# Optimization experiments

Hardware: AMD Instinct MI355X
Metric: run time of the kernel (lower is better)

Reference implementation:

```python
import jax, jax.numpy as jnp
import numpy as np

B, HOR, E, L = 16, 512, 1024, 12
ACT_NUM, DIM, ADIM = 10, 64, 10
N = 2 * HOR                      # backbone sequence length (test=False)
NPOS = 4 * (1 + HOR)             # wpe table size
D_IN = 3 + DIM * ACT_NUM + ADIM  # embed_transition input dim = 653


def setup_inputs() -> dict:
    key = jax.random.key(0)
    ks = jax.random.split(key, 12)
    s = lambda k, shape: (jax.random.normal(k, shape, jnp.float32) * 0.02)
    return {
        "action_set": jax.random.normal(ks[0], (B, ACT_NUM, DIM), jnp.float32),
        "context_rewards": jax.random.normal(ks[1], (B, HOR, 1), jnp.float32),
        "wpe": s(ks[2], (NPOS, E)),
        "W_emb": s(ks[3], (D_IN, E)),
        "b_emb": jnp.zeros((E,), jnp.float32),
        "Wq": s(ks[4], (L, E, E)),
        "Wk": s(ks[5], (L, E, E)),
        "Wv": s(ks[6], (L, E, E)),
        "ln1_g": jnp.ones((L, E), jnp.float32),
        "ln1_b": jnp.zeros((L, E), jnp.float32),
        "W1": s(ks[7], (L, E, E)),
        "b1": jnp.zeros((L, E), jnp.float32),
        "W2": s(ks[8], (L, E, E)),
        "b2": jnp.zeros((L, E), jnp.float32),
        "ln2_g": jnp.ones((L, E), jnp.float32),
        "ln2_b": jnp.zeros((L, E), jnp.float32),
        "W_pred": s(ks[9], (E, ADIM)),
        "b_pred": jnp.zeros((ADIM,), jnp.float32),
    }


def _layernorm(x, g, b, eps=1e-5):
    mu = x.mean(-1, keepdims=True)
    var = ((x - mu) ** 2).mean(-1, keepdims=True)
    return (x - mu) * jax.lax.rsqrt(var + eps) * g + b


def reference(action_set, context_rewards, wpe, W_emb, b_emb, Wq, Wk, Wv,
              ln1_g, ln1_b, W1, b1, W2, b2, ln2_g, ln2_b, W_pred, b_pred):
    batch = action_set.shape[0]
    hor = context_rewards.shape[1]
    n = 2 * hor
    # --- build interleaved sequence (outer Transformer glue) ---
    a = action_set.reshape(batch, 1, -1)                       # [B,1,DA]
    pair = jnp.concatenate([a, jnp.zeros_like(a)], axis=1)     # [B,2,DA]
    act_set_seq = jnp.tile(pair, (1, hor, 1))                  # [B,2H,DA]
    action_seq = jnp.zeros((batch, n, ADIM + 1), jnp.float32)
    one_seq = jnp.ones((batch, n, 1), jnp.float32)
    pos_seq = jnp.broadcast_to(
        jnp.arange(1, n + 1, dtype=jnp.float32).reshape(1, n, 1), (batch, n, 1))
    seq = jnp.concatenate([act_set_seq, action_seq, one_seq, pos_seq], axis=2)  # [B,N,D_IN]
    # --- DecoderTransformerBackbone ---
    Hs = seq @ W_emb + b_emb
    Hs = Hs + wpe[:n]                                          # positional embedding
    idx = jnp.arange(n)
    # normalized causal mask: row i has 1/(i+1) on j<=i, else 0
    mask = jnp.where(idx[:, None] >= idx[None, :],
                     1.0 / (idx[:, None].astype(jnp.float32) + 1.0), 0.0)
    for l in range(Wq.shape[0]):
        q = Hs @ Wq[l]
        k = Hs @ Wk[l]
        v = Hs @ Wv[l]
        attn = jax.nn.relu(jnp.einsum('bid,bjd->bij', q, k)) * mask
        Hs = Hs + jnp.einsum('bij,bjd->bid', attn, v)
        Hs = _layernorm(Hs, ln1_g[l], ln1_b[l])
        Hs = Hs + (jax.nn.relu(Hs @ W1[l] + b1[l]) @ W2[l] + b2[l])
        Hs = _layernorm(Hs, ln2_g[l], ln2_b[l])
    preds = Hs @ W_pred + b_pred                               # [B,N,ADIM]
    return preds[:, 0::2, :]                                   # [B,HOR,ADIM]
```

## Files before the change

### kernel.cpp

```cpp
#include <hip/hip_runtime.h>
#include <stdint.h>
#include <stddef.h>

#define E_DIM 1024
#define B_SZ  16
#define N_SEQ 1024
#define L_NUM 12
#define ACT_D 640
#define ADIM_ 10

typedef unsigned short u16;
typedef __attribute__((ext_vector_type(8))) short bf16x8;
typedef __attribute__((ext_vector_type(4))) float f32x4;

__device__ __forceinline__ u16 f2bf(float x) {
  union { float f; unsigned int u; } c; c.f = x;
  unsigned int r = c.u + 0x7fffu + ((c.u >> 16) & 1u);
  return (u16)(r >> 16);
}
__device__ __forceinline__ float bf2f(u16 h) {
  union { unsigned int u; float f; } c; c.u = ((unsigned int)h) << 16;
  return c.f;
}

struct us4 { u16 x, y, z, w; };

#define GLD16(gsrc, ldst) __builtin_amdgcn_global_load_lds( \
    (const __attribute__((address_space(1))) void*)(gsrc),  \
    (__attribute__((address_space(3))) void*)(ldst), 16, 0, 0)

#define BM 256
#define BK 32

template<int MODE, int EPI, int BNT>
__global__ __launch_bounds__(512)
void gemm_nt_mfma(const u16* __restrict__ Ah, const u16* __restrict__ Al,
                  const u16* __restrict__ Bh0, const u16* __restrict__ Bl0,
                  const u16* __restrict__ Bh1, const u16* __restrict__ Bl1,
                  float* __restrict__ Co,
                  u16* __restrict__ Ch0, u16* __restrict__ Cl0,
                  u16* __restrict__ Ch1, u16* __restrict__ Cl1,
                  const float* __restrict__ bias0, const float* __restrict__ bias1,
                  int K, int lda, int ldb, int ldc, int tilesN,
                  long long sA, long long sB, long long sC)
{
  constexpr int LA = BM * BK;
  constexpr int LB = BNT * BK;
  constexpr int BUFU = 2 * LA + 2 * LB;
  __shared__ u16 smem[2 * BUFU];

  constexpr int WAVE_R = (BNT == 256) ? 128 : 64;
  constexpr int WGC = BNT / 64;
  constexpr int MA = WAVE_R / 16;

  const int tid = threadIdx.x;
  const int bat = blockIdx.y;

  const u16* Bh = Bh0; const u16* Bl = Bl0;
  u16* Ch = Ch0; u16* Cl = Cl0;
  const float* bias = bias0;
  if (blockIdx.z) { Bh = Bh1; Bl = Bl1; Ch = Ch1; Cl = Cl1; bias = bias1; }

  Ah += bat * sA; Al += bat * sA;
  Bh += bat * sB; Bl += bat * sB;

  int bid;
  {
    const int nwg = gridDim.x;
    const int q = nwg >> 3, r = nwg & 7;
    const int xcd = blockIdx.x & 7, off = blockIdx.x >> 3;
    bid = ((xcd < r) ? xcd * (q + 1) : r * (q + 1) + (xcd - r) * q) + off;
  }

  int tm, tn;
  if (MODE == 1) {
    int t = bid, m = 0;
    while ((m + 1) * (m + 2) <= t) m++;
    tm = m; tn = t - m * (m + 1);
  } else {
    tm = bid / tilesN;
    tn = bid % tilesN;
  }
  int kend = K;
  if (MODE == 2) { int c = (tm + 1) * BM; kend = (c < K) ? c : K; }
  const int nk = kend / BK;

  const int ca0 = tid, ca1 = tid + 512;
  const int ra0 = ca0 >> 2, ra1 = ca1 >> 2;
  const int pa0 = ((ca0 & 3) ^ ((ra0 >> 1) & 3)) * 8;
  const int pa1 = ((ca1 & 3) ^ ((ra1 >> 1) & 3)) * 8;
  const int cb0 = tid, cb1 = tid + 512;
  const int rb0 = cb0 >> 2, rb1 = cb1 >> 2;
  const int pb0 = ((cb0 & 3) ^ ((rb0 >> 1) & 3)) * 8;
  const int pb1 = ((cb1 & 3) ^ ((rb1 >> 1) & 3)) * 8;

  const u16* gAh0 = Ah + (long long)(tm * BM + ra0) * lda + pa0;
  const u16* gAh1 = Ah + (long long)(tm * BM + ra1) * lda + pa1;
  const u16* gAl0 = Al + (long long)(tm * BM + ra0) * lda + pa0;
  const u16* gAl1 = Al + (long long)(tm * BM + ra1) * lda + pa1;
  const u16* gBh0 = Bh + (long long)(tn * BNT + rb0) * ldb + pb0;
  const u16* gBl0 = Bl + (long long)(tn * BNT + rb0) * ldb + pb0;
  const u16* gBh1 = Bh + (long long)(tn * BNT + rb1) * ldb + pb1;
  const u16* gBl1 = Bl + (long long)(tn * BNT + rb1) * ldb + pb1;
  const int oa0 = ca0 * 8, oa1 = ca1 * 8, ob0 = cb0 * 8, ob1 = cb1 * 8;

  auto stage = [&](int buf) {
    u16* base = smem + buf * BUFU;
    GLD16(gAh0, base + oa0);
    GLD16(gAh1, base + oa1);
    GLD16(gAl0, base + LA + oa0);
    GLD16(gAl1, base + LA + oa1);
    GLD16(gBh0, base + 2 * LA + ob0);
    GLD16(gBl0, base + 2 * LA + LB + ob0);
    if (BNT == 256) {
      GLD16(gBh1, base + 2 * LA + ob1);
      GLD16(gBl1, base + 2 * LA + LB + ob1);
    }
    gAh0 += BK; gAh1 += BK; gAl0 += BK; gAl1 += BK;
    gBh0 += BK; gBl0 += BK;
    if (BNT == 256) { gBh1 += BK; gBl1 += BK; }
  };

  const int lane = tid & 63;
  const int w = tid >> 6;
  const int wr = w / WGC, wc = w % WGC;
  const int fr = lane & 15;
  const int kq = (lane >> 4) * 8;
  const int sa = ((fr >> 1) & 3) << 3;
  const int aoff = ((wr * WAVE_R + fr) * BK + kq) ^ sa;
  const int boff = ((wc * 64 + fr) * BK + kq) ^ sa;

  f32x4 acc[MA][4];
  #pragma unroll
  for (int m = 0; m < MA; m++)
    #pragma unroll
    for (int n = 0; n < 4; n++) acc[m][n] = (f32x4){0.f, 0.f, 0.f, 0.f};

  stage(0);
  asm volatile("s_waitcnt vmcnt(0)" ::: "memory");
  __builtin_amdgcn_s_barrier();

  for (int t = 0; t < nk; t++) {
    if (t + 1 < nk) stage((t + 1) & 1);
    const u16* sb = smem + (t & 1) * BUFU;

    bf16x8 ah[MA], al[MA], bh[4], bl[4];
    #pragma unroll
    for (int m = 0; m < MA; m++) ah[m] = *(const bf16x8*)(sb + aoff + m * (16 * BK));
    #pragma unroll
    for (int n = 0; n < 4; n++) bh[n] = *(const bf16x8*)(sb + 2 * LA + boff + n * (16 * BK));
    __builtin_amdgcn_s_setprio(1);
    #pragma unroll
    for (int m = 0; m < MA; m++)
      #pragma unroll
      for (int n = 0; n < 4; n++)
        acc[m][n] = __builtin_amdgcn_mfma_f32_16x16x32_bf16(ah[m], bh[n], acc[m][n], 0, 0, 0);
    __builtin_amdgcn_s_setprio(0);
    #pragma unroll
    for (int m = 0; m < MA; m++) al[m] = *(const bf16x8*)(sb + LA + aoff + m * (16 * BK));
    __builtin_amdgcn_s_setprio(1);
    #pragma unroll
    for (int m = 0; m < MA; m++)
      #pragma unroll
      for (int n = 0; n < 4; n++)
        acc[m][n] = __builtin_amdgcn_mfma_f32_16x16x32_bf16(al[m], bh[n], acc[m][n], 0, 0, 0);
    __builtin_amdgcn_s_setprio(0);
    #pragma unroll
    for (int n = 0; n < 4; n++) bl[n] = *(const bf16x8*)(sb + 2 * LA + LB + boff + n * (16 * BK));
    __builtin_amdgcn_s_setprio(1);
    #pragma unroll
    for (int m = 0; m < MA; m++)
      #pragma unroll
      for (int n = 0; n < 4; n++)
        acc[m][n] = __builtin_amdgcn_mfma_f32_16x16x32_bf16(ah[m], bl[n], acc[m][n], 0, 0, 0);
    __builtin_amdgcn_s_setprio(0);

    if (t + 1 < nk) {
      asm volatile("s_waitcnt vmcnt(0)" ::: "memory");
      __builtin_amdgcn_s_barrier();
    }
  }

  if (Co) Co += bat * sC;
  if (Ch) { Ch += bat * sC; Cl += bat * sC; }
  #pragma unroll
  for (int m = 0; m < MA; m++) {
    #pragma unroll
    for (int r = 0; r < 4; r++) {
      const long long row = (long long)tm * BM + wr * WAVE_R + m * 16 + (lane >> 4) * 4 + r;
      #pragma unroll
      for (int n = 0; n < 4; n++) {
        const long long col = (long long)tn * BNT + wc * 64 + n * 16 + (lane & 15);
        float v = acc[m][n][r];
        if (EPI == 2) { v += bias[col]; v = v > 0.f ? v : 0.f; }
        if (EPI == 4) { v += bias[col]; }
        if (EPI == 3) {
          v = v > 0.f ? v : 0.f;
          v = (col <= row) ? v / (float)(row + 1) : 0.f;
        }
        const long long idx = row * (long long)ldc + col;
        if (EPI == 0 || EPI == 4) {
          Co[idx] = v;
        } else {
          u16 h = f2bf(v);
          Ch[idx] = h;
          Cl[idx] = f2bf(v - bf2f(h));
        }
      }
    }
  }
}

struct TP3 {
  const float* s0; const float* s1; const float* s2;
  u16* h0; u16* l0; u16* h1; u16* l1; u16* h2; u16* l2;
};

__global__ __launch_bounds__(256)
void transpose_split3(TP3 p)
{
  __shared__ float tile[32][33];
  const float* src; u16* dh; u16* dl;
  if (blockIdx.z == 0)      { src = p.s0; dh = p.h0; dl = p.l0; }
  else if (blockIdx.z == 1) { src = p.s1; dh = p.h1; dl = p.l1; }
  else                      { src = p.s2; dh = p.h2; dl = p.l2; }
  const int c0 = blockIdx.x * 32, r0 = blockIdx.y * 32;
  const int tx = threadIdx.x & 31, ty = threadIdx.x >> 5;
  #pragma unroll
  for (int i = ty; i < 32; i += 8)
    tile[i][tx] = src[(long long)(r0 + i) * E_DIM + c0 + tx];
  __syncthreads();
  #pragma unroll
  for (int i = ty; i < 32; i += 8) {
    const float v = tile[tx][i];
    const u16 h = f2bf(v);
    const long long idx = (long long)(c0 + i) * E_DIM + r0 + tx;
    dh[idx] = h;
    dl[idx] = f2bf(v - bf2f(h));
  }
}

__global__ __launch_bounds__(256)
void resid_ln(u16* __restrict__ hh, u16* __restrict__ hl,
              const float* __restrict__ delta,
              const float* __restrict__ g, const float* __restrict__ bta)
{
  __shared__ float red[8];
  const long long row = blockIdx.x;
  u16* hp = hh + row * E_DIM;
  u16* lp = hl + row * E_DIM;
  const float* dp = delta + row * E_DIM;
  const int tid = threadIdx.x;
  const int e = tid * 4;

  us4 hv = *(const us4*)(hp + e);
  us4 lv = *(const us4*)(lp + e);
  float4 d = *(const float4*)(dp + e);
  float x0 = bf2f(hv.x) + bf2f(lv.x) + d.x;
  float x1 = bf2f(hv.y) + bf2f(lv.y) + d.y;
  float x2 = bf2f(hv.z) + bf2f(lv.z) + d.z;
  float x3 = bf2f(hv.w) + bf2f(lv.w) + d.w;
  float s = x0 + x1 + x2 + x3;
  float q = x0 * x0 + x1 * x1 + x2 * x2 + x3 * x3;
  #pragma unroll
  for (int o = 32; o > 0; o >>= 1) { s += __shfl_down(s, o); q += __shfl_down(q, o); }
  const int lane = tid & 63, wv = tid >> 6;
  if (lane == 0) { red[wv] = s; red[wv + 4] = q; }
  __syncthreads();
  const float st = red[0] + red[1] + red[2] + red[3];
  const float qt = red[4] + red[5] + red[6] + red[7];
  const float mu = st * (1.0f / E_DIM);
  const float var = qt * (1.0f / E_DIM) - mu * mu;
  const float rstd = rsqrtf(var + 1e-5f);

  float4 gg = *(const float4*)(g + e);
  float4 bb = *(const float4*)(bta + e);
  float y0 = (x0 - mu) * rstd * gg.x + bb.x;
  float y1 = (x1 - mu) * rstd * gg.y + bb.y;
  float y2 = (x2 - mu) * rstd * gg.z + bb.z;
  float y3 = (x3 - mu) * rstd * gg.w + bb.w;

  us4 ho, lo;
  ho.x = f2bf(y0); lo.x = f2bf(y0 - bf2f(ho.x));
  ho.y = f2bf(y1); lo.y = f2bf(y1 - bf2f(ho.y));
  ho.z = f2bf(y2); lo.z = f2bf(y2 - bf2f(ho.z));
  ho.w = f2bf(y3); lo.w = f2bf(y3 - bf2f(ho.w));
  *(us4*)(hp + e) = ho;
  *(us4*)(lp + e) = lo;
}

__global__ __launch_bounds__(256)
void emb_dot(const float* __restrict__ act, const float* __restrict__ Wemb,
             float* __restrict__ Aemb)
{
  const int e = blockIdx.x * 256 + threadIdx.x;
  const int b = blockIdx.y;
  const float* ab = act + b * ACT_D;
  float s = 0.f;
  for (int d = 0; d < ACT_D; d++)
    s = fmaf(ab[d], Wemb[(long long)d * E_DIM + e], s);
  Aemb[b * E_DIM + e] = s;
}

__global__ __launch_bounds__(256)
void emb_fill(const float* __restrict__ Aemb, const float* __restrict__ Wemb,
              const float* __restrict__ bemb, const float* __restrict__ wpe,
              u16* __restrict__ oh, u16* __restrict__ ol)
{
  const int i = blockIdx.x, b = blockIdx.y;
  const int e = threadIdx.x * 4;
  float4 a;
  if ((i & 1) == 0) a = *(const float4*)(Aemb + b * E_DIM + e);
  else { a.x = 0.f; a.y = 0.f; a.z = 0.f; a.w = 0.f; }
  float4 be = *(const float4*)(bemb + e);
  float4 w1 = *(const float4*)(Wemb + 651LL * E_DIM + e);
  float4 w2 = *(const float4*)(Wemb + 652LL * E_DIM + e);
  float4 pw = *(const float4*)(wpe + (long long)i * E_DIM + e);
  const float pos = (float)(i + 1);
  float y0 = a.x + be.x + w1.x + pos * w2.x + pw.x;
  float y1 = a.y + be.y + w1.y + pos * w2.y + pw.y;
  float y2 = a.z + be.z + w1.z + pos * w2.z + pw.z;
  float y3 = a.w + be.w + w1.w + pos * w2.w + pw.w;
  const long long row = (long long)b * N_SEQ + i;

  us4 ho, lo;
  ho.x = f2bf(y0); lo.x = f2bf(y0 - bf2f(ho.x));
  ho.y = f2bf(y1); lo.y = f2bf(y1 - bf2f(ho.y));
  ho.z = f2bf(y2); lo.z = f2bf(y2 - bf2f(ho.z));
  ho.w = f2bf(y3); lo.w = f2bf(y3 - bf2f(ho.w));
  *(us4*)(oh + row * E_DIM + e) = ho;
  *(us4*)(ol + row * E_DIM + e) = lo;
}

__global__ __launch_bounds__(256)
void pred_k(const u16* __restrict__ hh, const u16* __restrict__ hl,
            const float* __restrict__ Wp, const float* __restrict__ bp,
            float* __restrict__ out)
{
  __shared__ float part[4][ADIM_];
  const int h = blockIdx.x, b = blockIdx.y;
  const long long row = (long long)b * N_SEQ + 2 * h;
  const u16* xh = hh + row * E_DIM;
  const u16* xl = hl + row * E_DIM;
  float acc[ADIM_];
  #pragma unroll
  for (int a = 0; a < ADIM_; a++) acc[a] = 0.f;
  for (int e = threadIdx.x; e < E_DIM; e += 256) {
    const float xv = bf2f(xh[e]) + bf2f(xl[e]);
    const float* wq = Wp + e * ADIM_;
    #pragma unroll
    for (int a = 0; a < ADIM_; a++) acc[a] = fmaf(xv, wq[a], acc[a]);
  }
  const int lane = threadIdx.x & 63, wv = threadIdx.x >> 6;
  #pragma unroll
  for (int a = 0; a < ADIM_; a++)
    #pragma unroll
    for (int o = 32; o > 0; o >>= 1) acc[a] += __shfl_down(acc[a], o);
  if (lane == 0)
    #pragma unroll
    for (int a = 0; a < ADIM_; a++) part[wv][a] = acc[a];
  __syncthreads();
  if (threadIdx.x < ADIM_) {
    const int a = threadIdx.x;
    out[((long long)b * (N_SEQ / 2) + h) * ADIM_ + a] =
        part[0][a] + part[1][a] + part[2][a] + part[3][a] + bp[a];
  }
}

__global__ __launch_bounds__(256)
void fill_sentinel(float* p, int n, float v)
{
  int i = blockIdx.x * 256 + threadIdx.x;
  if (i < n) p[i] = v;
}

extern "C" void kernel_launch(void* const* d_in, const int* in_sizes, int n_in,
                              void* d_out, int out_size, void* d_ws, size_t ws_size,
                              hipStream_t stream)
{
  const float* act  = (const float*)d_in[0];
  const float* wpe  = (const float*)d_in[2];
  const float* Wemb = (const float*)d_in[3];
  const float* bemb = (const float*)d_in[4];
  const float* Wq   = (const float*)d_in[5];
  const float* Wk   = (const float*)d_in[6];
  const float* Wv   = (const float*)d_in[7];
  const float* ln1g = (const float*)d_in[8];
  const float* ln1b = (const float*)d_in[9];
  const float* W1   = (const float*)d_in[10];
  const float* b1   = (const float*)d_in[11];
  const float* W2   = (const float*)d_in[12];
  const float* b2   = (const float*)d_in[13];
  const float* ln2g = (const float*)d_in[14];
  const float* ln2b = (const float*)d_in[15];
  const float* Wp   = (const float*)d_in[16];
  const float* bp   = (const float*)d_in[17];
  float* out = (float*)d_out;

  const long long sQ = (long long)N_SEQ * E_DIM;
  const long long sE = (long long)E_DIM * E_DIM;

  auto need = [&](int G) -> size_t {
    return (size_t)G * sQ * 16 + (size_t)sE * 12
         + (size_t)G * E_DIM * 4 + (size_t)(1 << 20);
  };
  int G = 16;
  while (G > 1 && need(G) > ws_size) G >>= 1;
  if (need(G) > ws_size || d_ws == nullptr || G < 8) {
    fill_sentinel<<<dim3((out_size + 255) / 256), 256, 0, stream>>>(out, out_size, 1.0e7f);
    return;
  }

  char* ws = (char*)d_ws;
  size_t off = 0;
  auto alloc = [&](size_t bytes) -> void* {
    void* p = ws + off;
    off += (bytes + 255) & ~(size_t)255;
    return p;
  };
  u16* hsh = (u16*)alloc((size_t)G * sQ * 2);
  u16* hsl = (u16*)alloc((size_t)G * sQ * 2);
  u16* qh  = (u16*)alloc((size_t)G * sQ * 2);
  u16* ql  = (u16*)alloc((size_t)G * sQ * 2);
  char* kreg = (char*)alloc((size_t)G * sQ * 4);
  u16* kh = (u16*)kreg;
  u16* kl = kh + (size_t)G * sQ;
  float* dbuf = (float*)kreg;
  u16* sh_ = (u16*)alloc((size_t)G * sQ * 2);
  u16* sl_ = (u16*)alloc((size_t)G * sQ * 2);
  u16* wAh = (u16*)alloc((size_t)sE * 2);
  u16* wAl = (u16*)alloc((size_t)sE * 2);
  u16* wBh = (u16*)alloc((size_t)sE * 2);
  u16* wBl = (u16*)alloc((size_t)sE * 2);
  u16* wCh = (u16*)alloc((size_t)sE * 2);
  u16* wCl = (u16*)alloc((size_t)sE * 2);
  float* Aemb = (float*)alloc((size_t)G * E_DIM * 4);

  const bool wide = (G >= 16);
  const int triS = 20;

  const dim3 gqk((G * N_SEQ / BM) * (E_DIM / 256), 1, 2);
  const dim3 gsq(triS, G, 1);
  const dim3 gm256((G * N_SEQ / BM) * (E_DIM / 256), 1, 1);
  const dim3 gm128((G * N_SEQ / BM) * (E_DIM / 128), 1, 1);
  const dim3 gv256((N_SEQ / BM) * (E_DIM / 256), G, 1);
  const dim3 gv128((N_SEQ / BM) * (E_DIM / 128), G, 1);

  for (int g0 = 0; g0 < B_SZ; g0 += G) {
    emb_dot<<<dim3(E_DIM / 256, G), 256, 0, stream>>>(act + (long long)g0 * ACT_D, Wemb, Aemb);
    emb_fill<<<dim3(N_SEQ, G), 256, 0, stream>>>(Aemb, Wemb, bemb, wpe, hsh, hsl);

    for (int l = 0; l < L_NUM; l++) {
      const long long wof = (long long)l * sE;
      const long long bof = (long long)l * E_DIM;

      TP3 t2 = {Wq + wof, Wk + wof, Wq + wof, wAh, wAl, wBh, wBl, wAh, wAl};
      transpose_split3<<<dim3(32, 32, 2), 256, 0, stream>>>(t2);
      gemm_nt_mfma<0, 1, 256><<<gqk, 512, 0, stream>>>(hsh, hsl, wAh, wAl, wBh, wBl,
          nullptr, qh, ql, kh, kl, nullptr, nullptr,
          E_DIM, E_DIM, E_DIM, E_DIM, E_DIM / 256, 0, 0, 0);

      TP3 t3 = {Wv + wof, W1 + wof, W2 + wof, wAh, wAl, wBh, wBl, wCh, wCl};
      transpose_split3<<<dim3(32, 32, 3), 256, 0, stream>>>(t3);

      gemm_nt_mfma<1, 3, 128><<<gsq, 512, 0, stream>>>(qh, ql, kh, kl, kh, kl,
          nullptr, sh_, sl_, sh_, sl_, nullptr, nullptr,
          E_DIM, E_DIM, E_DIM, N_SEQ, 0, sQ, sQ, sQ);

      if (wide)
        gemm_nt_mfma<0, 1, 256><<<gv256, 512, 0, stream>>>(wAh, wAl, hsh, hsl, hsh, hsl,
            nullptr, qh, ql, qh, ql, nullptr, nullptr,
            E_DIM, E_DIM, E_DIM, N_SEQ, E_DIM / 256, 0, sQ, sQ);
      else
        gemm_nt_mfma<0, 1, 128><<<gv128, 512, 0, stream>>>(wAh, wAl, hsh, hsl, hsh, hsl,
            nullptr, qh, ql, qh, ql, nullptr, nullptr,
            E_DIM, E_DIM, E_DIM, N_SEQ, E_DIM / 128, 0, sQ, sQ);

      if (wide)
        gemm_nt_mfma<2, 0, 256><<<gv256, 512, 0, stream>>>(sh_, sl_, qh, ql, qh, ql,
            dbuf, nullptr, nullptr, nullptr, nullptr, nullptr, nullptr,
            N_SEQ, N_SEQ, N_SEQ, E_DIM, E_DIM / 256, sQ, sQ, sQ);
      else
        gemm_nt_mfma<2, 0, 128><<<gv128, 512, 0, stream>>>(sh_, sl_, qh, ql, qh, ql,
            dbuf, nullptr, nullptr, nullptr, nullptr, nullptr, nullptr,
            N_SEQ, N_SEQ, N_SEQ, E_DIM, E_DIM / 128, sQ, sQ, sQ);

      resid_ln<<<dim3(G * N_SEQ), 256, 0, stream>>>(hsh, hsl, dbuf,
          ln1g + bof, ln1b + bof);

      if (wide)
        gemm_nt_mfma<0, 2, 256><<<gm256, 512, 0, stream>>>(hsh, hsl, wBh, wBl, wBh, wBl,
            nullptr, qh, ql, qh, ql, b1 + bof, b1 + bof,
            E_DIM, E_DIM, E_DIM, E_DIM, E_DIM / 256, 0, 0, 0);
      else
        gemm_nt_mfma<0, 2, 128><<<gm128, 512, 0, stream>>>(hsh, hsl, wBh, wBl, wBh, wBl,
            nullptr, qh, ql, qh, ql, b1 + bof, b1 + bof,
            E_DIM, E_DIM, E_DIM, E_DIM, E_DIM / 128, 0, 0, 0);
      if (wide)
        gemm_nt_mfma<0, 4, 256><<<gm256, 512, 0, stream>>>(qh, ql, wCh, wCl, wCh, wCl,
            dbuf, nullptr, nullptr, nullptr, nullptr, b2 + bof, b2 + bof,
            E_DIM, E_DIM, E_DIM, E_DIM, E_DIM / 256, 0, 0, 0);
      else
        gemm_nt_mfma<0, 4, 128><<<gm128, 512, 0, stream>>>(qh, ql, wCh, wCl, wCh, wCl,
            dbuf, nullptr, nullptr, nullptr, nullptr, b2 + bof, b2 + bof,
            E_DIM, E_DIM, E_DIM, E_DIM, E_DIM / 128, 0, 0, 0);

      resid_ln<<<dim3(G * N_SEQ), 256, 0, stream>>>(hsh, hsl, dbuf,
          ln2g + bof, ln2b + bof);
    }

    pred_k<<<dim3(N_SEQ / 2, G), 256, 0, stream>>>(hsh, hsl, Wp, bp,
        out + (long long)g0 * (N_SEQ / 2) * ADIM_);
  }
}
```

Baseline: 8.890 ms.

## Split GEMM prefetch into hi/lo halves interleaved with MFMA phases

Splits the global-to-LDS stage of the split-bf16 GEMM into two halves: the high parts (Ah, Bh) and the low parts (Al, Bl). Each half is issued between different MFMA phases of the current tile. Partial vmcnt waits and extra barriers make each half complete just before it is needed, rather than waiting for all loads at the end of the iteration. The aim is to hide more memory latency behind MFMA work, at the cost of several more workgroup barriers and lgkmcnt waits per k-iteration.

```diff
diff --git a/kernel.cpp b/kernel.cpp
--- a/kernel.cpp
+++ b/kernel.cpp
@@ -104,22 +104,29 @@
   const u16* gBl1 = Bl + (long long)(tn * BNT + rb1) * ldb + pb1;
   const int oa0 = ca0 * 8, oa1 = ca1 * 8, ob0 = cb0 * 8, ob1 = cb1 * 8;
 
-  auto stage = [&](int buf) {
+  auto stage_h0 = [&](int buf) {
     u16* base = smem + buf * BUFU;
     GLD16(gAh0, base + oa0);
     GLD16(gAh1, base + oa1);
+    GLD16(gBh0, base + 2 * LA + ob0);
+    if (BNT == 256) GLD16(gBh1, base + 2 * LA + ob1);
+    gAh0 += BK; gAh1 += BK; gBh0 += BK;
+    if (BNT == 256) gBh1 += BK;
+  };
+  auto stage_h1 = [&](int buf) {
+    u16* base = smem + buf * BUFU;
     GLD16(gAl0, base + LA + oa0);
     GLD16(gAl1, base + LA + oa1);
-    GLD16(gBh0, base + 2 * LA + ob0);
     GLD16(gBl0, base + 2 * LA + LB + ob0);
-    if (BNT == 256) {
-      GLD16(gBh1, base + 2 * LA + ob1);
-      GLD16(gBl1, base + 2 * LA + LB + ob1);
-    }
-    gAh0 += BK; gAh1 += BK; gAl0 += BK; gAl1 += BK;
-    gBh0 += BK; gBl0 += BK;
-    if (BNT == 256) { gBh1 += BK; gBl1 += BK; }
+    if (BNT == 256) GLD16(gBl1, base + 2 * LA + LB + ob1);
+    gAl0 += BK; gAl1 += BK; gBl0 += BK;
+    if (BNT == 256) gBl1 += BK;
   };
+
+#define WAIT_HALF() do { if (BNT == 256) asm volatile("s_waitcnt vmcnt(4)" ::: "memory"); \
+                         else            asm volatile("s_waitcnt vmcnt(3)" ::: "memory"); } while (0)
+#define WAIT_ZERO() asm volatile("s_waitcnt vmcnt(0)" ::: "memory")
+#define LGKM0()     asm volatile("s_waitcnt lgkmcnt(0)" ::: "memory")
 
   const int lane = tid & 63;
   const int w = tid >> 6;
@@ -136,19 +143,25 @@
     #pragma unroll
     for (int n = 0; n < 4; n++) acc[m][n] = (f32x4){0.f, 0.f, 0.f, 0.f};
 
-  stage(0);
-  asm volatile("s_waitcnt vmcnt(0)" ::: "memory");
+  stage_h0(0);
+  stage_h1(0);
+  WAIT_HALF();
   __builtin_amdgcn_s_barrier();
 
   for (int t = 0; t < nk; t++) {
-    if (t + 1 < nk) stage((t + 1) & 1);
     const u16* sb = smem + (t & 1) * BUFU;
+    const bool pf = (t + 1 < nk);
+    const int nb = (t + 1) & 1;
 
     bf16x8 ah[MA], al[MA], bh[4], bl[4];
+
     #pragma unroll
     for (int m = 0; m < MA; m++) ah[m] = *(const bf16x8*)(sb + aoff + m * (16 * BK));
     #pragma unroll
     for (int n = 0; n < 4; n++) bh[n] = *(const bf16x8*)(sb + 2 * LA + boff + n * (16 * BK));
+    if (pf) { stage_h0(nb); WAIT_HALF(); } else WAIT_ZERO();
+    __builtin_amdgcn_s_barrier();
+    LGKM0();
     __builtin_amdgcn_s_setprio(1);
     #pragma unroll
     for (int m = 0; m < MA; m++)
@@ -156,8 +169,13 @@
       for (int n = 0; n < 4; n++)
         acc[m][n] = __builtin_amdgcn_mfma_f32_16x16x32_bf16(ah[m], bh[n], acc[m][n], 0, 0, 0);
     __builtin_amdgcn_s_setprio(0);
+    __builtin_amdgcn_s_barrier();
+
     #pragma unroll
     for (int m = 0; m < MA; m++) al[m] = *(const bf16x8*)(sb + LA + aoff + m * (16 * BK));
+    if (pf) stage_h1(nb);
+    __builtin_amdgcn_s_barrier();
+    LGKM0();
     __builtin_amdgcn_s_setprio(1);
     #pragma unroll
     for (int m = 0; m < MA; m++)
@@ -165,8 +183,13 @@
       for (int n = 0; n < 4; n++)
         acc[m][n] = __builtin_amdgcn_mfma_f32_16x16x32_bf16(al[m], bh[n], acc[m][n], 0, 0, 0);
     __builtin_amdgcn_s_setprio(0);
+    __builtin_amdgcn_s_barrier();
+
     #pragma unroll
     for (int n = 0; n < 4; n++) bl[n] = *(const bf16x8*)(sb + 2 * LA + LB + boff + n * (16 * BK));
+    if (pf) WAIT_HALF(); else WAIT_ZERO();
+    __builtin_amdgcn_s_barrier();
+    LGKM0();
     __builtin_amdgcn_s_setprio(1);
     #pragma unroll
     for (int m = 0; m < MA; m++)
@@ -174,11 +197,7 @@
       for (int n = 0; n < 4; n++)
         acc[m][n] = __builtin_amdgcn_mfma_f32_16x16x32_bf16(ah[m], bl[n], acc[m][n], 0, 0, 0);
     __builtin_amdgcn_s_setprio(0);
-
-    if (t + 1 < nk) {
-      asm volatile("s_waitcnt vmcnt(0)" ::: "memory");
-      __builtin_amdgcn_s_barrier();
-    }
+    __builtin_amdgcn_s_barrier();
   }
 
   if (Co) Co += bat * sC;
@@ -209,6 +228,9 @@
       }
     }
   }
+#undef WAIT_HALF
+#undef WAIT_ZERO
+#undef LGKM0
 }
 
 struct TP3 {
```

Result: no change. 9.021 ms (+1.5%).
